# Performance work log

Measured on AMD Instinct MI355X. Metric: run time of the kernel, lower is better.

The kernel has to match this reference:

```python
import jax, jax.numpy as jnp
import numpy as np

DIM = 2048        # config.dim
HID = 1408        # config.moe_inter_dim
E = 16            # config.n_routed_experts
TOPK = 4          # config.n_activated_experts
SHARED = 2816     # n_shared_experts * moe_inter_dim
B, S = 1, 2048
ROUTE_SCALE = 1.0


def setup_inputs() -> dict:
    key = jax.random.key(0)
    ks = jax.random.split(key, 8)
    def w(k, shape, fan_in):
        return jax.random.normal(k, shape, jnp.float32) * (1.0 / np.sqrt(fan_in))
    return {
        "x": jax.random.normal(ks[0], (B, S, DIM), jnp.float32),
        "gate_w": w(ks[1], (E, DIM), DIM),
        "w1": w(ks[2], (E, HID, DIM), DIM),   # per-expert nn.Linear(dim, hid).weight
        "w2": w(ks[3], (E, DIM, HID), HID),   # per-expert nn.Linear(hid, dim).weight
        "w3": w(ks[4], (E, HID, DIM), DIM),
        "sw1": w(ks[5], (SHARED, DIM), DIM),  # shared MLP weights
        "sw2": w(ks[6], (DIM, SHARED), SHARED),
        "sw3": w(ks[7], (SHARED, DIM), DIM),
    }


def reference(x, gate_w, w1, w2, w3, sw1, sw2, sw3):
    shape = x.shape
    xt = x.reshape(-1, DIM)                      # [T, D]
    T = xt.shape[0]

    # --- Gate (score_func='softmax', n_groups=1, bias=None since dim != 7168) ---
    logits = xt @ gate_w.T                        # [T, E]
    scores = jax.nn.softmax(logits.astype(jnp.float32), axis=-1)
    topv, idx = jax.lax.top_k(scores, TOPK)       # n_groups==1: topk over flat scores
    weights = topv * ROUTE_SCALE                  # gather(original_scores, idx) == topv here

    # aux load-balance loss
    tpe = jnp.zeros((E,), jnp.float32).at[idx.reshape(-1)].add(1.0) / (T * TOPK)
    aux_loss = E * jnp.sum(tpe * scores.mean(axis=0))

    # --- Routed experts: combine weights [T, E], then batched SwiGLU GEMMs ---
    comb = jnp.zeros((T, E), jnp.float32).at[jnp.arange(T)[:, None], idx].add(weights)
    h = jax.nn.silu(jnp.einsum('td,ehd->teh', xt, w1)) * jnp.einsum('td,ehd->teh', xt, w3)
    y = jnp.einsum('teh,edh,te->td', h, w2, comb)  # weighted combine (0-weight experts cancel)

    # --- Shared experts (SwiGLU MLP, dropout=0) ---
    z = (jax.nn.silu(xt @ sw1.T) * (xt @ sw3.T)) @ sw2.T

    return (y + z).reshape(shape), aux_loss
```

## Files before the change

kernel.cpp:

```cpp
#include <hip/hip_runtime.h>
#include <hip/hip_bf16.h>

typedef unsigned short u16;
typedef __attribute__((ext_vector_type(8))) short short8;
typedef __attribute__((ext_vector_type(4))) float f32x4;

#define DIM 2048
#define HID 1408
#define NE 16
#define NTOK 2048
#define TOPK_ 4
#define SHID 2816
#define CAPROWS 10240
#define MAXTILES (CAPROWS / 128)
#define AUX_IDX (2048 * 2048)

__device__ inline u16 f2bf(float f) {
  __bf16 h = (__bf16)f;
  return __builtin_bit_cast(u16, h);
}

__device__ inline void gload_lds16(const void* g, void* l) {
  __builtin_amdgcn_global_load_lds(
      (const __attribute__((address_space(1))) unsigned int*)g,
      (__attribute__((address_space(3))) unsigned int*)l, 16, 0, 0);
}

__global__ __launch_bounds__(256) void gate_dots_kernel(
    const float* __restrict__ x, const float* __restrict__ gw,
    double* __restrict__ logits) {
  int t = blockIdx.x;
  const float* xt = x + (size_t)t * DIM;
  __shared__ double red[NE][4];
  int lane = threadIdx.x & 63, wid = threadIdx.x >> 6;
  for (int e = 0; e < NE; ++e) {
    const float* w = gw + e * DIM;
    double p = 0.0;
    for (int d = threadIdx.x; d < DIM; d += 256)
      p += (double)xt[d] * (double)w[d];
#pragma unroll
    for (int s = 32; s; s >>= 1) p += __shfl_xor(p, s);
    if (lane == 0) red[e][wid] = p;
  }
  __syncthreads();
  if (threadIdx.x < NE) {
    int e = threadIdx.x;
    logits[(size_t)t * NE + e] = red[e][0] + red[e][1] + red[e][2] + red[e][3];
  }
}

__global__ __launch_bounds__(256) void topk_kernel(
    const double* __restrict__ logits,
    int* __restrict__ idxb, float* __restrict__ wtb,
    int* __restrict__ counts, float* __restrict__ ssum) {
  __shared__ int lcnt[NE];
  __shared__ float lsum[NE];
  if (threadIdx.x < NE) { lcnt[threadIdx.x] = 0; lsum[threadIdx.x] = 0.f; }
  __syncthreads();
  int t = blockIdx.x * 256 + threadIdx.x;
  int lane = threadIdx.x & 63;
  double sc[NE];
  double m = -1e300;
#pragma unroll
  for (int e = 0; e < NE; ++e) {
    sc[e] = logits[(size_t)t * NE + e];
    if (sc[e] > m) m = sc[e];
  }
  double s = 0.0;
#pragma unroll
  for (int e = 0; e < NE; ++e) { sc[e] = exp(sc[e] - m); s += sc[e]; }
  double inv = 1.0 / s;
#pragma unroll
  for (int e = 0; e < NE; ++e) sc[e] *= inv;
  unsigned used = 0;
  for (int k = 0; k < TOPK_; ++k) {
    int be = 0; double bv = -1.0;
#pragma unroll
    for (int e = 0; e < NE; ++e)
      if (!((used >> e) & 1u) && sc[e] > bv) { bv = sc[e]; be = e; }
    used |= 1u << be;
    idxb[t * TOPK_ + k] = be;
    wtb[t * TOPK_ + k] = (float)bv;
    atomicAdd(&lcnt[be], 1);
  }
#pragma unroll
  for (int e = 0; e < NE; ++e) {
    float v = (float)sc[e];
#pragma unroll
    for (int sft = 32; sft; sft >>= 1) v += __shfl_xor(v, sft);
    if (lane == 0) atomicAdd(&lsum[e], v);
  }
  __syncthreads();
  if (threadIdx.x < NE) {
    atomicAdd(&counts[threadIdx.x], lcnt[threadIdx.x]);
    atomicAdd(&ssum[threadIdx.x], lsum[threadIdx.x]);
  }
}

__global__ __launch_bounds__(256) void setup_kernel(
    const int* __restrict__ counts, int* __restrict__ off, int* __restrict__ cap,
    const float* __restrict__ ssum, int* __restrict__ perm, float* __restrict__ pwt,
    float* __restrict__ aux_out,
    int* __restrict__ tile2e, int* __restrict__ tile2m0) {
  for (int i = threadIdx.x; i < MAXTILES; i += 256) tile2e[i] = -1;
  __syncthreads();
  if (threadIdx.x == 0) {
    int o = 0; double aux = 0.0; int nt = 0;
    for (int e = 0; e < NE; ++e) {
      off[e] = o;
      int c = (counts[e] + 127) & ~127;
      cap[e] = c;
      for (int t = 0; t < (c >> 7); ++t) {
        int slot = (nt / 10) + (nt % 10) * 8;
        tile2e[slot] = e;
        tile2m0[slot] = o + t * 128;
        ++nt;
      }
      o += c;
      aux += ((double)counts[e] / (NTOK * TOPK_)) * ((double)ssum[e] / NTOK);
    }
    aux_out[0] = (float)(NE * aux);
  }
  for (int i = threadIdx.x; i < CAPROWS; i += 256) { perm[i] = 0; pwt[i] = 0.f; }
}

__global__ __launch_bounds__(256) void scatter_kernel(
    const int* __restrict__ idxb, const float* __restrict__ wtb,
    const int* __restrict__ off, int* __restrict__ cursor,
    int* __restrict__ perm, float* __restrict__ pwt) {
  int t = blockIdx.x * 256 + threadIdx.x;
  if (t >= NTOK) return;
  for (int k = 0; k < TOPK_; ++k) {
    int e = idxb[t * TOPK_ + k];
    int s = atomicAdd(&cursor[e], 1);
    int p = off[e] + s;
    perm[p] = t;
    pwt[p] = wtb[t * TOPK_ + k];
  }
}

__global__ __launch_bounds__(256) void cvtN_kernel(const float* __restrict__ in,
                                                   u16* __restrict__ out, long n) {
  long stride = (long)gridDim.x * 2048;
  for (long i = ((long)blockIdx.x * 256 + threadIdx.x) * 8; i < n; i += stride) {
    float4 a = *(const float4*)(in + i);
    float4 b = *(const float4*)(in + i + 4);
    union { u16 u[8]; uint4 v; } o;
    o.u[0] = f2bf(a.x); o.u[1] = f2bf(a.y); o.u[2] = f2bf(a.z); o.u[3] = f2bf(a.w);
    o.u[4] = f2bf(b.x); o.u[5] = f2bf(b.y); o.u[6] = f2bf(b.z); o.u[7] = f2bf(b.w);
    *(uint4*)(out + i) = o.v;
  }
}

template <bool GATHER, bool DUAL, int EPI>
__global__ __launch_bounds__(256) void gemm9_kernel(
    const u16* __restrict__ A, int lda,
    const float* __restrict__ B1, const float* __restrict__ B3,
    int ldb, long bstride, int K,
    const int* __restrict__ tile2e, const int* __restrict__ tile2m0,
    const int* __restrict__ seg_off, const int* __restrict__ seg_cnt,
    const int* __restrict__ perm, const float* __restrict__ pwt,
    float* __restrict__ C0, int ldc0,
    u16* __restrict__ Cb, int ldcb, int Mfixed) {
  int e, m0, rowlim;
  if (tile2e) {
    e = tile2e[blockIdx.x];
    if (e < 0) return;
    m0 = tile2m0[blockIdx.x];
    rowlim = seg_off[e] + seg_cnt[e];
  } else {
    e = 0;
    m0 = blockIdx.x * 128;
    if (m0 >= Mfixed) return;
    rowlim = Mfixed;
  }
  int n0 = blockIdx.y * 64;
  const float* Bb1 = B1 + (long)e * bstride;
  const float* Bb3 = DUAL ? (B3 + (long)e * bstride) : nullptr;

  __shared__ u16 As[2][128 * 64];
  __shared__ u16 Bs1[64 * 64];
  __shared__ u16 Bs3[DUAL ? 64 * 64 : 1];

  int tid = threadIdx.x;
  int lane = tid & 63;
  int wid = tid >> 6;
  int wr = wid >> 1, wc = wid & 1;

  f32x4 acc1[4][2], acc3[4][2];
#pragma unroll
  for (int mi = 0; mi < 4; ++mi)
#pragma unroll
    for (int ni = 0; ni < 2; ++ni) {
      acc1[mi][ni] = (f32x4){0.f, 0.f, 0.f, 0.f};
      acc3[mi][ni] = (f32x4){0.f, 0.f, 0.f, 0.f};
    }

  int sr = tid >> 3;
  int scA = tid & 7;
  long abase[4];
#pragma unroll
  for (int it = 0; it < 4; ++it) {
    int row = m0 + it * 32 + sr;
    int rid = GATHER ? perm[row] : row;
    abase[it] = (long)rid * lda + ((scA ^ (sr & 7)) << 3);
  }
  int brr = tid >> 4;
  int gB = tid & 15;
  int wofs = (((gB >> 1) ^ (brr & 7)) << 3) + ((gB & 1) << 2);
  long bbase[4];
#pragma unroll
  for (int it = 0; it < 4; ++it)
    bbase[it] = (long)(n0 + it * 16 + brr) * ldb + gB * 4;

  float4 R1a[4], R3a[4], R1b[4], R3b[4];

  auto stageA = [&](int buf, int k0) {
#pragma unroll
    for (int it = 0; it < 4; ++it)
      gload_lds16(A + abase[it] + k0, &As[buf][(it * 32 + sr) * 64 + scA * 8]);
  };
  auto loadB = [&](float4 (&r1)[4], float4 (&r3)[4], int k0) {
#pragma unroll
    for (int it = 0; it < 4; ++it) r1[it] = *(const float4*)(Bb1 + bbase[it] + k0);
    if (DUAL) {
#pragma unroll
      for (int it = 0; it < 4; ++it) r3[it] = *(const float4*)(Bb3 + bbase[it] + k0);
    }
  };
  auto writeB = [&](float4 (&r1)[4], float4 (&r3)[4]) {
#pragma unroll
    for (int it = 0; it < 4; ++it) {
      int lo = (it * 16 + brr) * 64 + wofs;
      ushort4 o;
      o.x = f2bf(r1[it].x); o.y = f2bf(r1[it].y); o.z = f2bf(r1[it].z); o.w = f2bf(r1[it].w);
      *(ushort4*)&Bs1[lo] = o;
      if (DUAL) {
        ushort4 q;
        q.x = f2bf(r3[it].x); q.y = f2bf(r3[it].y); q.z = f2bf(r3[it].z); q.w = f2bf(r3[it].w);
        *(ushort4*)&Bs3[lo] = q;
      }
    }
  };
  auto compute = [&](int cur) {
#pragma unroll
    for (int kk = 0; kk < 64; kk += 32) {
      short8 af[4], b1f[2], b3f[2];
#pragma unroll
      for (int i = 0; i < 4; ++i) {
        int R = wr * 64 + i * 16 + (lane & 15);
        int c = (kk >> 3) + (lane >> 4);
        af[i] = *(const short8*)&As[cur][R * 64 + ((c ^ (R & 7)) << 3)];
      }
#pragma unroll
      for (int i = 0; i < 2; ++i) {
        int r = wc * 32 + i * 16 + (lane & 15);
        int cR = (kk >> 3) + (lane >> 4);
        b1f[i] = *(const short8*)&Bs1[r * 64 + ((cR ^ (r & 7)) << 3)];
        if (DUAL)
          b3f[i] = *(const short8*)&Bs3[r * 64 + ((cR ^ (r & 7)) << 3)];
      }
#pragma unroll
      for (int mi = 0; mi < 4; ++mi)
#pragma unroll
        for (int ni = 0; ni < 2; ++ni) {
          acc1[mi][ni] = __builtin_amdgcn_mfma_f32_16x16x32_bf16(af[mi], b1f[ni], acc1[mi][ni], 0, 0, 0);
          if (DUAL)
            acc3[mi][ni] = __builtin_amdgcn_mfma_f32_16x16x32_bf16(af[mi], b3f[ni], acc3[mi][ni], 0, 0, 0);
        }
    }
  };

  int NT = K >> 6;
  loadB(R1a, R3a, 0);
  stageA(0, 0);
  loadB(R1b, R3b, 64);

#define GEMM9_STEP(T, CUR, RB1, RB3)                                          \
  {                                                                           \
    int t_ = (T);                                                             \
    writeB(RB1, RB3);                           \
    bool hasA = (t_ + 1 < NT), hasB = (t_ + 2 < NT);                          \
    if (hasA) stageA((CUR) ^ 1, (t_ + 1) << 6);                               \
    if (hasB) loadB(RB1, RB3, (t_ + 2) << 6);                                 \
    if (hasB) {                                                               \
      if (DUAL) asm volatile("s_waitcnt vmcnt(20)" ::: "memory");             \
      else      asm volatile("s_waitcnt vmcnt(12)" ::: "memory");             \
    } else if (hasA) {                                                        \
      if (DUAL) asm volatile("s_waitcnt vmcnt(12)" ::: "memory");             \
      else      asm volatile("s_waitcnt vmcnt(8)"  ::: "memory");             \
    } else {                                                                  \
      asm volatile("s_waitcnt vmcnt(0)" ::: "memory");                        \
    }                                                                         \
    asm volatile("s_waitcnt lgkmcnt(0)" ::: "memory");                        \
    __builtin_amdgcn_sched_barrier(0);                                        \
    __builtin_amdgcn_s_barrier();                    \
    __builtin_amdgcn_sched_barrier(0);                                        \
    compute(CUR);                                                             \
    __builtin_amdgcn_sched_barrier(0);                                        \
    __builtin_amdgcn_s_barrier();           \
  }

  for (int t = 0; t < NT; t += 2) {
    GEMM9_STEP(t,     0, R1a, R3a);
    GEMM9_STEP(t + 1, 1, R1b, R3b);
  }
#undef GEMM9_STEP

  int rbase = m0 + wr * 64 + (lane >> 4) * 4;
  int cbase = n0 + wc * 32 + (lane & 15);
#pragma unroll
  for (int mi = 0; mi < 4; ++mi) {
#pragma unroll
    for (int ni = 0; ni < 2; ++ni) {
      int col = cbase + ni * 16;
#pragma unroll
      for (int r = 0; r < 4; ++r) {
        int row = rbase + mi * 16 + r;
        float v = acc1[mi][ni][r];
        if (EPI == 0) {
          float a3 = acc3[mi][ni][r];
          float sg = v / (1.f + __expf(-v));
          Cb[(long)row * ldcb + col] = f2bf(sg * a3);
        } else if (EPI == 1) {
          C0[(long)row * ldc0 + col] = v;
        } else {
          if (row < rowlim) {
            atomicAdd(&C0[(long)perm[row] * ldc0 + col], v * pwt[row]);
          }
        }
      }
    }
  }
}

extern "C" void kernel_launch(void* const* d_in, const int* in_sizes, int n_in,
                              void* d_out, int out_size, void* d_ws, size_t ws_size,
                              hipStream_t stream) {
  (void)in_sizes; (void)n_in; (void)out_size; (void)ws_size;
  const float* x   = (const float*)d_in[0];
  const float* gw  = (const float*)d_in[1];
  const float* w1  = (const float*)d_in[2];
  const float* w2  = (const float*)d_in[3];
  const float* w3  = (const float*)d_in[4];
  const float* sw1 = (const float*)d_in[5];
  const float* sw2 = (const float*)d_in[6];
  const float* sw3 = (const float*)d_in[7];
  float* out = (float*)d_out;
  char* ws = (char*)d_ws;

  int*   counts = (int*)(ws + 0);
  int*   cursor = (int*)(ws + 64);
  int*   off    = (int*)(ws + 128);
  int*   cap    = (int*)(ws + 192);
  float* ssum   = (float*)(ws + 256);
  int*   tile2e = (int*)(ws + 1024);
  int*   tile2m0= (int*)(ws + 2048);
  int*   idxb   = (int*)(ws + 4096);
  float* wtb    = (float*)(ws + 4096 + 32768);
  int*   perm   = (int*)(ws + 4096 + 65536);
  float* pwt    = (float*)(ws + 4096 + 65536 + 40960);
  u16*   xb     = (u16*)(ws + 262144);
  double* logits = (double*)(ws + 8650752);
  u16*   hbuf   = (u16*)(ws + 16777216);
  u16*   hsb    = (u16*)(ws + 45613056);

  hipMemsetAsync(ws, 0, 512, stream);
  gate_dots_kernel<<<dim3(NTOK), dim3(256), 0, stream>>>(x, gw, logits);
  topk_kernel<<<dim3(NTOK / 256), dim3(256), 0, stream>>>(logits, idxb, wtb, counts, ssum);
  setup_kernel<<<dim3(1), dim3(256), 0, stream>>>(counts, off, cap, ssum, perm, pwt,
                                                  out + AUX_IDX, tile2e, tile2m0);
  scatter_kernel<<<dim3(8), dim3(256), 0, stream>>>(idxb, wtb, off, cursor, perm, pwt);
  cvtN_kernel<<<dim3(2048), dim3(256), 0, stream>>>(x, xb, (long)NTOK * DIM);

  gemm9_kernel<true, true, 0><<<dim3(MAXTILES, HID / 64), dim3(256), 0, stream>>>(
      xb, DIM, w1, w3, DIM, (long)HID * DIM, DIM, tile2e, tile2m0,
      off, counts, perm, pwt, nullptr, 0, hbuf, HID, 0);
  gemm9_kernel<false, true, 0><<<dim3(NTOK / 128, SHID / 64), dim3(256), 0, stream>>>(
      xb, DIM, sw1, sw3, DIM, 0, DIM, nullptr, nullptr,
      nullptr, nullptr, nullptr, nullptr, nullptr, 0, hsb, SHID, NTOK);
  gemm9_kernel<false, false, 1><<<dim3(NTOK / 128, DIM / 64), dim3(256), 0, stream>>>(
      hsb, SHID, sw2, nullptr, SHID, 0, SHID, nullptr, nullptr,
      nullptr, nullptr, nullptr, nullptr, out, DIM, nullptr, 0, NTOK);
  gemm9_kernel<false, false, 2><<<dim3(MAXTILES, DIM / 64), dim3(256), 0, stream>>>(
      hbuf, HID, w2, nullptr, HID, (long)DIM * HID, HID, tile2e, tile2m0,
      off, counts, perm, pwt, out, DIM, nullptr, 0, 0);
}
```

Baseline: 604.0 us.

## Pre-convert routed expert weights to bf16 and stream them via direct LDS loads

When the workspace is large enough, the routed expert weights w1/w3 (and later w2) are converted to bf16 once. The w1/w3 conversion is folded into the gate-logit kernel as extra blocks, and the w2 conversion runs in spare blocks of the shared-expert GEMM. A new GEMM variant then loads bf16 B tiles with global_load_lds into double-buffered LDS, replacing the register-staged fp32 load and convert path. This adds a full extra read and write pass over the expert weights each call in exchange for halving the per-tile weight traffic and simplifying the pipeline. The w3 branch stores each converted chunk twice through a redundant expression.

```diff
diff --git a/kernel.cpp b/kernel.cpp
--- a/kernel.cpp
+++ b/kernel.cpp
@@ -14,6 +14,8 @@
 #define CAPROWS 10240
 #define MAXTILES (CAPROWS / 128)
 #define AUX_IDX (2048 * 2048)
+#define NW13 46137344L
+#define NX 4194304L
 
 __device__ inline u16 f2bf(float f) {
   __bf16 h = (__bf16)f;
@@ -26,9 +28,31 @@
       (__attribute__((address_space(3))) unsigned int*)l, 16, 0, 0);
 }
 
-__global__ __launch_bounds__(256) void gate_dots_kernel(
+__device__ inline void cvt8_store(const float* __restrict__ in, u16* __restrict__ out, long i) {
+  float4 a = *(const float4*)(in + i);
+  float4 b = *(const float4*)(in + i + 4);
+  union { u16 u[8]; uint4 v; } o;
+  o.u[0] = f2bf(a.x); o.u[1] = f2bf(a.y); o.u[2] = f2bf(a.z); o.u[3] = f2bf(a.w);
+  o.u[4] = f2bf(b.x); o.u[5] = f2bf(b.y); o.u[6] = f2bf(b.z); o.u[7] = f2bf(b.w);
+  *(uint4*)(out + i) = o.v;
+}
+
+__global__ __launch_bounds__(256) void prep_kernel(
     const float* __restrict__ x, const float* __restrict__ gw,
-    double* __restrict__ logits) {
+    double* __restrict__ logits,
+    const float* __restrict__ w1, const float* __restrict__ w3,
+    u16* __restrict__ w1b, u16* __restrict__ w3b, u16* __restrict__ xb) {
+  if ((int)blockIdx.x >= NTOK) {
+    long i0 = ((long)(blockIdx.x - NTOK) * 256 + threadIdx.x) * 8;
+    long stride = (long)(gridDim.x - NTOK) * 2048;
+    const long ntot = 2 * NW13 + NX;
+    for (long i = i0; i < ntot; i += stride) {
+      if (i < NW13)            cvt8_store(w1, w1b, i);
+      else if (i < 2 * NW13)   cvt8_store(w3 + (i - NW13) - (i - NW13), w3b, i - NW13), cvt8_store(w3, w3b, i - NW13);
+      else                     cvt8_store(x, xb, i - 2 * NW13);
+    }
+    return;
+  }
   int t = blockIdx.x;
   const float* xt = x + (size_t)t * DIM;
   __shared__ double red[NE][4];
@@ -43,10 +67,9 @@
     if (lane == 0) red[e][wid] = p;
   }
   __syncthreads();
-  if (threadIdx.x < NE) {
-    int e = threadIdx.x;
-    logits[(size_t)t * NE + e] = red[e][0] + red[e][1] + red[e][2] + red[e][3];
-  }
+  if (threadIdx.x < NE)
+    logits[(size_t)t * NE + threadIdx.x] =
+        red[threadIdx.x][0] + red[threadIdx.x][1] + red[threadIdx.x][2] + red[threadIdx.x][3];
 }
 
 __global__ __launch_bounds__(256) void topk_kernel(
@@ -142,20 +165,202 @@
 __global__ __launch_bounds__(256) void cvtN_kernel(const float* __restrict__ in,
                                                    u16* __restrict__ out, long n) {
   long stride = (long)gridDim.x * 2048;
-  for (long i = ((long)blockIdx.x * 256 + threadIdx.x) * 8; i < n; i += stride) {
-    float4 a = *(const float4*)(in + i);
-    float4 b = *(const float4*)(in + i + 4);
-    union { u16 u[8]; uint4 v; } o;
-    o.u[0] = f2bf(a.x); o.u[1] = f2bf(a.y); o.u[2] = f2bf(a.z); o.u[3] = f2bf(a.w);
-    o.u[4] = f2bf(b.x); o.u[5] = f2bf(b.y); o.u[6] = f2bf(b.z); o.u[7] = f2bf(b.w);
-    *(uint4*)(out + i) = o.v;
-  }
+  for (long i = ((long)blockIdx.x * 256 + threadIdx.x) * 8; i < n; i += stride)
+    cvt8_store(in, out, i);
 }
 
 template <bool GATHER, bool DUAL, int EPI>
 __global__ __launch_bounds__(256) void gemm9_kernel(
     const u16* __restrict__ A, int lda,
     const float* __restrict__ B1, const float* __restrict__ B3,
+    int ldb, long bstride, int K,
+    const int* __restrict__ tile2e, const int* __restrict__ tile2m0,
+    const int* __restrict__ seg_off, const int* __restrict__ seg_cnt,
+    const int* __restrict__ perm, const float* __restrict__ pwt,
+    float* __restrict__ C0, int ldc0,
+    u16* __restrict__ Cb, int ldcb, int Mfixed,
+    const float* __restrict__ csrc, u16* __restrict__ cdst, long cn, int nxg) {
+  if ((int)blockIdx.x >= nxg) {
+    long i0 = ((long)((blockIdx.x - nxg) * gridDim.y + blockIdx.y) * 256 + threadIdx.x) * 8;
+    long stride = (long)(gridDim.x - nxg) * gridDim.y * 2048;
+    for (long i = i0; i < cn; i += stride) cvt8_store(csrc, cdst, i);
+    return;
+  }
+  int e, m0, rowlim;
+  if (tile2e) {
+    e = tile2e[blockIdx.x];
+    if (e < 0) return;
+    m0 = tile2m0[blockIdx.x];
+    rowlim = seg_off[e] + seg_cnt[e];
+  } else {
+    e = 0;
+    m0 = blockIdx.x * 128;
+    if (m0 >= Mfixed) return;
+    rowlim = Mfixed;
+  }
+  int n0 = blockIdx.y * 64;
+  const float* Bb1 = B1 + (long)e * bstride;
+  const float* Bb3 = DUAL ? (B3 + (long)e * bstride) : nullptr;
+
+  __shared__ u16 As[2][128 * 64];
+  __shared__ u16 Bs1[64 * 64];
+  __shared__ u16 Bs3[DUAL ? 64 * 64 : 1];
+
+  int tid = threadIdx.x;
+  int lane = tid & 63;
+  int wid = tid >> 6;
+  int wr = wid >> 1, wc = wid & 1;
+
+  f32x4 acc1[4][2], acc3[4][2];
+#pragma unroll
+  for (int mi = 0; mi < 4; ++mi)
+#pragma unroll
+    for (int ni = 0; ni < 2; ++ni) {
+      acc1[mi][ni] = (f32x4){0.f, 0.f, 0.f, 0.f};
+      acc3[mi][ni] = (f32x4){0.f, 0.f, 0.f, 0.f};
+    }
+
+  int sr = tid >> 3;
+  int scA = tid & 7;
+  long abase[4];
+#pragma unroll
+  for (int it = 0; it < 4; ++it) {
+    int row = m0 + it * 32 + sr;
+    int rid = GATHER ? perm[row] : row;
+    abase[it] = (long)rid * lda + ((scA ^ (sr & 7)) << 3);
+  }
+  int brr = tid >> 4;
+  int gB = tid & 15;
+  int wofs = (((gB >> 1) ^ (brr & 7)) << 3) + ((gB & 1) << 2);
+  long bbase[4];
+#pragma unroll
+  for (int it = 0; it < 4; ++it)
+    bbase[it] = (long)(n0 + it * 16 + brr) * ldb + gB * 4;
+
+  float4 R1a[4], R3a[4], R1b[4], R3b[4];
+
+  auto stageA = [&](int buf, int k0) {
+#pragma unroll
+    for (int it = 0; it < 4; ++it)
+      gload_lds16(A + abase[it] + k0, &As[buf][(it * 32 + sr) * 64 + scA * 8]);
+  };
+  auto loadB = [&](float4 (&r1)[4], float4 (&r3)[4], int k0) {
+#pragma unroll
+    for (int it = 0; it < 4; ++it) r1[it] = *(const float4*)(Bb1 + bbase[it] + k0);
+    if (DUAL) {
+#pragma unroll
+      for (int it = 0; it < 4; ++it) r3[it] = *(const float4*)(Bb3 + bbase[it] + k0);
+    }
+  };
+  auto writeB = [&](float4 (&r1)[4], float4 (&r3)[4]) {
+#pragma unroll
+    for (int it = 0; it < 4; ++it) {
+      int lo = (it * 16 + brr) * 64 + wofs;
+      ushort4 o;
+      o.x = f2bf(r1[it].x); o.y = f2bf(r1[it].y); o.z = f2bf(r1[it].z); o.w = f2bf(r1[it].w);
+      *(ushort4*)&Bs1[lo] = o;
+      if (DUAL) {
+        ushort4 q;
+        q.x = f2bf(r3[it].x); q.y = f2bf(r3[it].y); q.z = f2bf(r3[it].z); q.w = f2bf(r3[it].w);
+        *(ushort4*)&Bs3[lo] = q;
+      }
+    }
+  };
+  auto compute = [&](int cur) {
+#pragma unroll
+    for (int kk = 0; kk < 64; kk += 32) {
+      short8 af[4], b1f[2], b3f[2];
+#pragma unroll
+      for (int i = 0; i < 4; ++i) {
+        int R = wr * 64 + i * 16 + (lane & 15);
+        int c = (kk >> 3) + (lane >> 4);
+        af[i] = *(const short8*)&As[cur][R * 64 + ((c ^ (R & 7)) << 3)];
+      }
+#pragma unroll
+      for (int i = 0; i < 2; ++i) {
+        int r = wc * 32 + i * 16 + (lane & 15);
+        int cR = (kk >> 3) + (lane >> 4);
+        b1f[i] = *(const short8*)&Bs1[r * 64 + ((cR ^ (r & 7)) << 3)];
+        if (DUAL)
+          b3f[i] = *(const short8*)&Bs3[r * 64 + ((cR ^ (r & 7)) << 3)];
+      }
+#pragma unroll
+      for (int mi = 0; mi < 4; ++mi)
+#pragma unroll
+        for (int ni = 0; ni < 2; ++ni) {
+          acc1[mi][ni] = __builtin_amdgcn_mfma_f32_16x16x32_bf16(af[mi], b1f[ni], acc1[mi][ni], 0, 0, 0);
+          if (DUAL)
+            acc3[mi][ni] = __builtin_amdgcn_mfma_f32_16x16x32_bf16(af[mi], b3f[ni], acc3[mi][ni], 0, 0, 0);
+        }
+    }
+  };
+
+  int NT = K >> 6;
+  loadB(R1a, R3a, 0);
+  stageA(0, 0);
+  loadB(R1b, R3b, 64);
+
+#define GEMM9_STEP(T, CUR, RB1, RB3)                                          \
+  {                                                                           \
+    int t_ = (T);                                                             \
+    writeB(RB1, RB3);                                                         \
+    bool hasA = (t_ + 1 < NT), hasB = (t_ + 2 < NT);                          \
+    if (hasA) stageA((CUR) ^ 1, (t_ + 1) << 6);                               \
+    if (hasB) loadB(RB1, RB3, (t_ + 2) << 6);                                 \
+    if (hasB) {                                                               \
+      if (DUAL) asm volatile("s_waitcnt vmcnt(20)" ::: "memory");             \
+      else      asm volatile("s_waitcnt vmcnt(12)" ::: "memory");             \
+    } else if (hasA) {                                                        \
+      if (DUAL) asm volatile("s_waitcnt vmcnt(12)" ::: "memory");             \
+      else      asm volatile("s_waitcnt vmcnt(8)"  ::: "memory");             \
+    } else {                                                                  \
+      asm volatile("s_waitcnt vmcnt(0)" ::: "memory");                        \
+    }                                                                         \
+    asm volatile("s_waitcnt lgkmcnt(0)" ::: "memory");                        \
+    __builtin_amdgcn_sched_barrier(0);                                        \
+    __builtin_amdgcn_s_barrier();                                             \
+    __builtin_amdgcn_sched_barrier(0);                                        \
+    compute(CUR);                                                             \
+    __builtin_amdgcn_sched_barrier(0);                                        \
+    __builtin_amdgcn_s_barrier();                                             \
+  }
+
+  for (int t = 0; t < NT; t += 2) {
+    GEMM9_STEP(t,     0, R1a, R3a);
+    GEMM9_STEP(t + 1, 1, R1b, R3b);
+  }
+#undef GEMM9_STEP
+
+  int rbase = m0 + wr * 64 + (lane >> 4) * 4;
+  int cbase = n0 + wc * 32 + (lane & 15);
+#pragma unroll
+  for (int mi = 0; mi < 4; ++mi) {
+#pragma unroll
+    for (int ni = 0; ni < 2; ++ni) {
+      int col = cbase + ni * 16;
+#pragma unroll
+      for (int r = 0; r < 4; ++r) {
+        int row = rbase + mi * 16 + r;
+        float v = acc1[mi][ni][r];
+        if (EPI == 0) {
+          float a3 = acc3[mi][ni][r];
+          float sg = v / (1.f + __expf(-v));
+          Cb[(long)row * ldcb + col] = f2bf(sg * a3);
+        } else if (EPI == 1) {
+          C0[(long)row * ldc0 + col] = v;
+        } else {
+          if (row < rowlim)
+            atomicAdd(&C0[(long)perm[row] * ldc0 + col], v * pwt[row]);
+        }
+      }
+    }
+  }
+}
+
+template <bool GATHER, bool DUAL, int EPI>
+__global__ __launch_bounds__(256) void gemm11_kernel(
+    const u16* __restrict__ A, int lda,
+    const u16* __restrict__ B1, const u16* __restrict__ B3,
     int ldb, long bstride, int K,
     const int* __restrict__ tile2e, const int* __restrict__ tile2m0,
     const int* __restrict__ seg_off, const int* __restrict__ seg_cnt,
@@ -175,12 +380,12 @@
     rowlim = Mfixed;
   }
   int n0 = blockIdx.y * 64;
-  const float* Bb1 = B1 + (long)e * bstride;
-  const float* Bb3 = DUAL ? (B3 + (long)e * bstride) : nullptr;
+  const u16* Bb1 = B1 + (long)e * bstride;
+  const u16* Bb3 = DUAL ? (B3 + (long)e * bstride) : nullptr;
 
   __shared__ u16 As[2][128 * 64];
-  __shared__ u16 Bs1[64 * 64];
-  __shared__ u16 Bs3[DUAL ? 64 * 64 : 1];
+  __shared__ u16 Bs1[2][64 * 64];
+  __shared__ u16 Bs3[DUAL ? 2 : 1][DUAL ? 64 * 64 : 1];
 
   int tid = threadIdx.x;
   int lane = tid & 63;
@@ -205,41 +410,22 @@
     int rid = GATHER ? perm[row] : row;
     abase[it] = (long)rid * lda + ((scA ^ (sr & 7)) << 3);
   }
-  int brr = tid >> 4;
-  int gB = tid & 15;
-  int wofs = (((gB >> 1) ^ (brr & 7)) << 3) + ((gB & 1) << 2);
-  long bbase[4];
-#pragma unroll
-  for (int it = 0; it < 4; ++it)
-    bbase[it] = (long)(n0 + it * 16 + brr) * ldb + gB * 4;
-
-  float4 R1a[4], R3a[4], R1b[4], R3b[4];
-
-  auto stageA = [&](int buf, int k0) {
+  long bbase[2];
+#pragma unroll
+  for (int it = 0; it < 2; ++it)
+    bbase[it] = (long)(n0 + it * 32 + sr) * ldb + ((scA ^ (sr & 7)) << 3);
+
+  auto stage = [&](int buf, int k0) {
 #pragma unroll
     for (int it = 0; it < 4; ++it)
       gload_lds16(A + abase[it] + k0, &As[buf][(it * 32 + sr) * 64 + scA * 8]);
-  };
-  auto loadB = [&](float4 (&r1)[4], float4 (&r3)[4], int k0) {
-#pragma unroll
-    for (int it = 0; it < 4; ++it) r1[it] = *(const float4*)(Bb1 + bbase[it] + k0);
+#pragma unroll
+    for (int it = 0; it < 2; ++it)
+      gload_lds16(Bb1 + bbase[it] + k0, &Bs1[buf][(it * 32 + sr) * 64 + scA * 8]);
     if (DUAL) {
 #pragma unroll
-      for (int it = 0; it < 4; ++it) r3[it] = *(const float4*)(Bb3 + bbase[it] + k0);
-    }
-  };
-  auto writeB = [&](float4 (&r1)[4], float4 (&r3)[4]) {
-#pragma unroll
-    for (int it = 0; it < 4; ++it) {
-      int lo = (it * 16 + brr) * 64 + wofs;
-      ushort4 o;
-      o.x = f2bf(r1[it].x); o.y = f2bf(r1[it].y); o.z = f2bf(r1[it].z); o.w = f2bf(r1[it].w);
-      *(ushort4*)&Bs1[lo] = o;
-      if (DUAL) {
-        ushort4 q;
-        q.x = f2bf(r3[it].x); q.y = f2bf(r3[it].y); q.z = f2bf(r3[it].z); q.w = f2bf(r3[it].w);
-        *(ushort4*)&Bs3[lo] = q;
-      }
+      for (int it = 0; it < 2; ++it)
+        gload_lds16(Bb3 + bbase[it] + k0, &Bs3[buf][(it * 32 + sr) * 64 + scA * 8]);
     }
   };
   auto compute = [&](int cur) {
@@ -256,9 +442,9 @@
       for (int i = 0; i < 2; ++i) {
         int r = wc * 32 + i * 16 + (lane & 15);
         int cR = (kk >> 3) + (lane >> 4);
-        b1f[i] = *(const short8*)&Bs1[r * 64 + ((cR ^ (r & 7)) << 3)];
+        b1f[i] = *(const short8*)&Bs1[cur][r * 64 + ((cR ^ (r & 7)) << 3)];
         if (DUAL)
-          b3f[i] = *(const short8*)&Bs3[r * 64 + ((cR ^ (r & 7)) << 3)];
+          b3f[i] = *(const short8*)&Bs3[cur][r * 64 + ((cR ^ (r & 7)) << 3)];
       }
 #pragma unroll
       for (int mi = 0; mi < 4; ++mi)
@@ -271,41 +457,27 @@
     }
   };
 
+  stage(0, 0);
   int NT = K >> 6;
-  loadB(R1a, R3a, 0);
-  stageA(0, 0);
-  loadB(R1b, R3b, 64);
-
-#define GEMM9_STEP(T, CUR, RB1, RB3)                                          \
-  {                                                                           \
-    int t_ = (T);                                                             \
-    writeB(RB1, RB3);                           \
-    bool hasA = (t_ + 1 < NT), hasB = (t_ + 2 < NT);                          \
-    if (hasA) stageA((CUR) ^ 1, (t_ + 1) << 6);                               \
-    if (hasB) loadB(RB1, RB3, (t_ + 2) << 6);                                 \
-    if (hasB) {                                                               \
-      if (DUAL) asm volatile("s_waitcnt vmcnt(20)" ::: "memory");             \
-      else      asm volatile("s_waitcnt vmcnt(12)" ::: "memory");             \
-    } else if (hasA) {                                                        \
-      if (DUAL) asm volatile("s_waitcnt vmcnt(12)" ::: "memory");             \
-      else      asm volatile("s_waitcnt vmcnt(8)"  ::: "memory");             \
-    } else {                                                                  \
-      asm volatile("s_waitcnt vmcnt(0)" ::: "memory");                        \
-    }                                                                         \
-    asm volatile("s_waitcnt lgkmcnt(0)" ::: "memory");                        \
-    __builtin_amdgcn_sched_barrier(0);                                        \
-    __builtin_amdgcn_s_barrier();                    \
-    __builtin_amdgcn_sched_barrier(0);                                        \
-    compute(CUR);                                                             \
-    __builtin_amdgcn_sched_barrier(0);                                        \
-    __builtin_amdgcn_s_barrier();           \
-  }
-
-  for (int t = 0; t < NT; t += 2) {
-    GEMM9_STEP(t,     0, R1a, R3a);
-    GEMM9_STEP(t + 1, 1, R1b, R3b);
-  }
-#undef GEMM9_STEP
+  int cur = 0;
+  for (int t = 0; t < NT; ++t) {
+    int nxt = cur ^ 1;
+    bool pf = (t + 1 < NT);
+    if (pf) {
+      stage(nxt, (t + 1) << 6);
+      if (DUAL) asm volatile("s_waitcnt vmcnt(8)" ::: "memory");
+      else      asm volatile("s_waitcnt vmcnt(6)" ::: "memory");
+    } else {
+      asm volatile("s_waitcnt vmcnt(0)" ::: "memory");
+    }
+    __builtin_amdgcn_sched_barrier(0);
+    __builtin_amdgcn_s_barrier();
+    __builtin_amdgcn_sched_barrier(0);
+    compute(cur);
+    __builtin_amdgcn_sched_barrier(0);
+    __builtin_amdgcn_s_barrier();
+    cur = nxt;
+  }
 
   int rbase = m0 + wr * 64 + (lane >> 4) * 4;
   int cbase = n0 + wc * 32 + (lane & 15);
@@ -325,9 +497,8 @@
         } else if (EPI == 1) {
           C0[(long)row * ldc0 + col] = v;
         } else {
-          if (row < rowlim) {
+          if (row < rowlim)
             atomicAdd(&C0[(long)perm[row] * ldc0 + col], v * pwt[row]);
-          }
         }
       }
     }
@@ -337,7 +508,7 @@
 extern "C" void kernel_launch(void* const* d_in, const int* in_sizes, int n_in,
                               void* d_out, int out_size, void* d_ws, size_t ws_size,
                               hipStream_t stream) {
-  (void)in_sizes; (void)n_in; (void)out_size; (void)ws_size;
+  (void)in_sizes; (void)n_in; (void)out_size;
   const float* x   = (const float*)d_in[0];
   const float* gw  = (const float*)d_in[1];
   const float* w1  = (const float*)d_in[2];
@@ -364,25 +535,56 @@
   double* logits = (double*)(ws + 8650752);
   u16*   hbuf   = (u16*)(ws + 16777216);
   u16*   hsb    = (u16*)(ws + 45613056);
+  u16*   w1b    = (u16*)(ws + 57147392);
+  u16*   w3b    = (u16*)(ws + 149422080);
+  u16*   w2b    = w1b;
+
+  const size_t NEEDED = 241696768ull;
+  bool bf16w = ws_size >= NEEDED;
 
   hipMemsetAsync(ws, 0, 512, stream);
-  gate_dots_kernel<<<dim3(NTOK), dim3(256), 0, stream>>>(x, gw, logits);
-  topk_kernel<<<dim3(NTOK / 256), dim3(256), 0, stream>>>(logits, idxb, wtb, counts, ssum);
-  setup_kernel<<<dim3(1), dim3(256), 0, stream>>>(counts, off, cap, ssum, perm, pwt,
-                                                  out + AUX_IDX, tile2e, tile2m0);
-  scatter_kernel<<<dim3(8), dim3(256), 0, stream>>>(idxb, wtb, off, cursor, perm, pwt);
-  cvtN_kernel<<<dim3(2048), dim3(256), 0, stream>>>(x, xb, (long)NTOK * DIM);
-
-  gemm9_kernel<true, true, 0><<<dim3(MAXTILES, HID / 64), dim3(256), 0, stream>>>(
-      xb, DIM, w1, w3, DIM, (long)HID * DIM, DIM, tile2e, tile2m0,
-      off, counts, perm, pwt, nullptr, 0, hbuf, HID, 0);
-  gemm9_kernel<false, true, 0><<<dim3(NTOK / 128, SHID / 64), dim3(256), 0, stream>>>(
-      xb, DIM, sw1, sw3, DIM, 0, DIM, nullptr, nullptr,
-      nullptr, nullptr, nullptr, nullptr, nullptr, 0, hsb, SHID, NTOK);
-  gemm9_kernel<false, false, 1><<<dim3(NTOK / 128, DIM / 64), dim3(256), 0, stream>>>(
-      hsb, SHID, sw2, nullptr, SHID, 0, SHID, nullptr, nullptr,
-      nullptr, nullptr, nullptr, nullptr, out, DIM, nullptr, 0, NTOK);
-  gemm9_kernel<false, false, 2><<<dim3(MAXTILES, DIM / 64), dim3(256), 0, stream>>>(
-      hbuf, HID, w2, nullptr, HID, (long)DIM * HID, HID, tile2e, tile2m0,
-      off, counts, perm, pwt, out, DIM, nullptr, 0, 0);
-}
+
+  if (bf16w) {
+    prep_kernel<<<dim3(NTOK + 1536), dim3(256), 0, stream>>>(x, gw, logits, w1, w3, w1b, w3b, xb);
+    topk_kernel<<<dim3(NTOK / 256), dim3(256), 0, stream>>>(logits, idxb, wtb, counts, ssum);
+    setup_kernel<<<dim3(1), dim3(256), 0, stream>>>(counts, off, cap, ssum, perm, pwt,
+                                                    out + AUX_IDX, tile2e, tile2m0);
+    scatter_kernel<<<dim3(8), dim3(256), 0, stream>>>(idxb, wtb, off, cursor, perm, pwt);
+
+    gemm11_kernel<true, true, 0><<<dim3(MAXTILES, HID / 64), dim3(256), 0, stream>>>(
+        xb, DIM, w1b, w3b, DIM, (long)HID * DIM, DIM, tile2e, tile2m0,
+        off, counts, perm, pwt, nullptr, 0, hbuf, HID, 0);
+    gemm9_kernel<false, true, 0><<<dim3(16 + 8, SHID / 64), dim3(256), 0, stream>>>(
+        xb, DIM, sw1, sw3, DIM, 0, DIM, nullptr, nullptr,
+        nullptr, nullptr, nullptr, nullptr, nullptr, 0, hsb, SHID, NTOK,
+        w2, w2b, NW13, 16);
+    gemm9_kernel<false, false, 1><<<dim3(NTOK / 128, DIM / 64), dim3(256), 0, stream>>>(
+        hsb, SHID, sw2, nullptr, SHID, 0, SHID, nullptr, nullptr,
+        nullptr, nullptr, nullptr, nullptr, out, DIM, nullptr, 0, NTOK,
+        nullptr, nullptr, 0, 1 << 30);
+    gemm11_kernel<false, false, 2><<<dim3(MAXTILES, DIM / 64), dim3(256), 0, stream>>>(
+        hbuf, HID, w2b, nullptr, HID, (long)DIM * HID, HID, tile2e, tile2m0,
+        off, counts, perm, pwt, out, DIM, nullptr, 0, 0);
+  } else {
+    prep_kernel<<<dim3(NTOK), dim3(256), 0, stream>>>(x, gw, logits, w1, w3, nullptr, nullptr, nullptr);
+    topk_kernel<<<dim3(NTOK / 256), dim3(256), 0, stream>>>(logits, idxb, wtb, counts, ssum);
+    setup_kernel<<<dim3(1), dim3(256), 0, stream>>>(counts, off, cap, ssum, perm, pwt,
+                                                    out + AUX_IDX, tile2e, tile2m0);
+    scatter_kernel<<<dim3(8), dim3(256), 0, stream>>>(idxb, wtb, off, cursor, perm, pwt);
+    cvtN_kernel<<<dim3(2048), dim3(256), 0, stream>>>(x, xb, (long)NTOK * DIM);
+    gemm9_kernel<true, true, 0><<<dim3(MAXTILES, HID / 64), dim3(256), 0, stream>>>(
+        xb, DIM, w1, w3, DIM, (long)HID * DIM, DIM, tile2e, tile2m0,
+        off, counts, perm, pwt, nullptr, 0, hbuf, HID, 0, nullptr, nullptr, 0, 1 << 30);
+    gemm9_kernel<false, true, 0><<<dim3(NTOK / 128, SHID / 64), dim3(256), 0, stream>>>(
+        xb, DIM, sw1, sw3, DIM, 0, DIM, nullptr, nullptr,
+        nullptr, nullptr, nullptr, nullptr, nullptr, 0, hsb, SHID, NTOK,
+        nullptr, nullptr, 0, 1 << 30);
+    gemm9_kernel<false, false, 1><<<dim3(NTOK / 128, DIM / 64), dim3(256), 0, stream>>>(
+        hsb, SHID, sw2, nullptr, SHID, 0, SHID, nullptr, nullptr,
+        nullptr, nullptr, nullptr, nullptr, out, DIM, nullptr, 0, NTOK,
+        nullptr, nullptr, 0, 1 << 30);
+    gemm9_kernel<false, false, 2><<<dim3(MAXTILES, DIM / 64), dim3(256), 0, stream>>>(
+        hbuf, HID, w2, nullptr, HID, (long)DIM * HID, HID, tile2e, tile2m0,
+        off, counts, perm, pwt, out, DIM, nullptr, 0, 0, nullptr, nullptr, 0, 1 << 30);
+  }
+}
```

Measured after the change: 726.6 us. 1.2x slower.

## Merge routed and shared expert GEMMs into combined launches, fuse cvt into gate

Applied to the files above, without the earlier changes.

Runs the routed-expert and shared-expert up-projection GEMMs as one launch with a role split on blockIdx.x, and does the same for the down-projections. All down-projection outputs are atomically accumulated into an output buffer that is zeroed by a memset beforehand. The bf16 conversion of x is folded into extra blocks of the gate-dot kernel. The aim is to cut launch count and tail underutilisation by letting independent GEMMs fill the GPU together. The cost is a full-output memset plus atomic adds for the shared path, and MAXTILES is cut from 80 slots to 80 (NSLOT 88), which could truncate routed tiles if the setup kernel assumes the old count.

```diff
diff --git a/kernel.cpp b/kernel.cpp
--- a/kernel.cpp
+++ b/kernel.cpp
@@ -12,7 +12,8 @@
 #define TOPK_ 4
 #define SHID 2816
 #define CAPROWS 10240
-#define MAXTILES (CAPROWS / 128)
+#define NSLOT 88
+#define MAXTILES 80
 #define AUX_IDX (2048 * 2048)
 
 __device__ inline u16 f2bf(float f) {
@@ -26,9 +27,24 @@
       (__attribute__((address_space(3))) unsigned int*)l, 16, 0, 0);
 }
 
-__global__ __launch_bounds__(256) void gate_dots_kernel(
+__device__ inline void cvt8_store(const float* __restrict__ in, u16* __restrict__ out, long i) {
+  float4 a = *(const float4*)(in + i);
+  float4 b = *(const float4*)(in + i + 4);
+  union { u16 u[8]; uint4 v; } o;
+  o.u[0] = f2bf(a.x); o.u[1] = f2bf(a.y); o.u[2] = f2bf(a.z); o.u[3] = f2bf(a.w);
+  o.u[4] = f2bf(b.x); o.u[5] = f2bf(b.y); o.u[6] = f2bf(b.z); o.u[7] = f2bf(b.w);
+  *(uint4*)(out + i) = o.v;
+}
+
+__global__ __launch_bounds__(256) void gatecvt_kernel(
     const float* __restrict__ x, const float* __restrict__ gw,
-    double* __restrict__ logits) {
+    double* __restrict__ logits, u16* __restrict__ xb) {
+  if ((int)blockIdx.x >= NTOK) {
+    long i0 = ((long)(blockIdx.x - NTOK) * 256 + threadIdx.x) * 8;
+    long stride = (long)(gridDim.x - NTOK) * 2048;
+    for (long i = i0; i < (long)NTOK * DIM; i += stride) cvt8_store(x, xb, i);
+    return;
+  }
   int t = blockIdx.x;
   const float* xt = x + (size_t)t * DIM;
   __shared__ double red[NE][4];
@@ -43,10 +59,9 @@
     if (lane == 0) red[e][wid] = p;
   }
   __syncthreads();
-  if (threadIdx.x < NE) {
-    int e = threadIdx.x;
-    logits[(size_t)t * NE + e] = red[e][0] + red[e][1] + red[e][2] + red[e][3];
-  }
+  if (threadIdx.x < NE)
+    logits[(size_t)t * NE + threadIdx.x] =
+        red[threadIdx.x][0] + red[threadIdx.x][1] + red[threadIdx.x][2] + red[threadIdx.x][3];
 }
 
 __global__ __launch_bounds__(256) void topk_kernel(
@@ -139,48 +154,41 @@
   }
 }
 
-__global__ __launch_bounds__(256) void cvtN_kernel(const float* __restrict__ in,
-                                                   u16* __restrict__ out, long n) {
-  long stride = (long)gridDim.x * 2048;
-  for (long i = ((long)blockIdx.x * 256 + threadIdx.x) * 8; i < n; i += stride) {
-    float4 a = *(const float4*)(in + i);
-    float4 b = *(const float4*)(in + i + 4);
-    union { u16 u[8]; uint4 v; } o;
-    o.u[0] = f2bf(a.x); o.u[1] = f2bf(a.y); o.u[2] = f2bf(a.z); o.u[3] = f2bf(a.w);
-    o.u[4] = f2bf(b.x); o.u[5] = f2bf(b.y); o.u[6] = f2bf(b.z); o.u[7] = f2bf(b.w);
-    *(uint4*)(out + i) = o.v;
-  }
-}
-
-template <bool GATHER, bool DUAL, int EPI>
-__global__ __launch_bounds__(256) void gemm9_kernel(
-    const u16* __restrict__ A, int lda,
-    const float* __restrict__ B1, const float* __restrict__ B3,
-    int ldb, long bstride, int K,
+__global__ __launch_bounds__(256) void gemmP1_kernel(
+    const u16* __restrict__ xb,
+    const float* __restrict__ w1, const float* __restrict__ w3,
+    const float* __restrict__ sw1, const float* __restrict__ sw3,
+    u16* __restrict__ hbuf, u16* __restrict__ hsb,
     const int* __restrict__ tile2e, const int* __restrict__ tile2m0,
-    const int* __restrict__ seg_off, const int* __restrict__ seg_cnt,
-    const int* __restrict__ perm, const float* __restrict__ pwt,
-    float* __restrict__ C0, int ldc0,
-    u16* __restrict__ Cb, int ldcb, int Mfixed) {
-  int e, m0, rowlim;
-  if (tile2e) {
-    e = tile2e[blockIdx.x];
+    const int* __restrict__ perm) {
+  int x = blockIdx.x, y = blockIdx.y;
+  bool shared_role = (x >= NSLOT);
+  int m0;
+  bool gth;
+  const float *Bb1, *Bb3;
+  u16* Cb;
+  int ldcb;
+  if (!shared_role) {
+    if (y >= HID / 64) return;
+    int e = tile2e[x];
     if (e < 0) return;
-    m0 = tile2m0[blockIdx.x];
-    rowlim = seg_off[e] + seg_cnt[e];
+    m0 = tile2m0[x];
+    gth = true;
+    Bb1 = w1 + (long)e * HID * DIM;
+    Bb3 = w3 + (long)e * HID * DIM;
+    Cb = hbuf; ldcb = HID;
   } else {
-    e = 0;
-    m0 = blockIdx.x * 128;
-    if (m0 >= Mfixed) return;
-    rowlim = Mfixed;
-  }
-  int n0 = blockIdx.y * 64;
-  const float* Bb1 = B1 + (long)e * bstride;
-  const float* Bb3 = DUAL ? (B3 + (long)e * bstride) : nullptr;
+    m0 = (x - NSLOT) * 128;
+    gth = false;
+    Bb1 = sw1; Bb3 = sw3;
+    Cb = hsb; ldcb = SHID;
+  }
+  int n0 = y * 64;
+  const int K = DIM, ldb = DIM, lda = DIM;
 
   __shared__ u16 As[2][128 * 64];
   __shared__ u16 Bs1[64 * 64];
-  __shared__ u16 Bs3[DUAL ? 64 * 64 : 1];
+  __shared__ u16 Bs3[64 * 64];
 
   int tid = threadIdx.x;
   int lane = tid & 63;
@@ -202,7 +210,7 @@
 #pragma unroll
   for (int it = 0; it < 4; ++it) {
     int row = m0 + it * 32 + sr;
-    int rid = GATHER ? perm[row] : row;
+    int rid = gth ? perm[row] : row;
     abase[it] = (long)rid * lda + ((scA ^ (sr & 7)) << 3);
   }
   int brr = tid >> 4;
@@ -218,15 +226,13 @@
   auto stageA = [&](int buf, int k0) {
 #pragma unroll
     for (int it = 0; it < 4; ++it)
-      gload_lds16(A + abase[it] + k0, &As[buf][(it * 32 + sr) * 64 + scA * 8]);
+      gload_lds16(xb + abase[it] + k0, &As[buf][(it * 32 + sr) * 64 + scA * 8]);
   };
   auto loadB = [&](float4 (&r1)[4], float4 (&r3)[4], int k0) {
 #pragma unroll
     for (int it = 0; it < 4; ++it) r1[it] = *(const float4*)(Bb1 + bbase[it] + k0);
-    if (DUAL) {
-#pragma unroll
-      for (int it = 0; it < 4; ++it) r3[it] = *(const float4*)(Bb3 + bbase[it] + k0);
-    }
+#pragma unroll
+    for (int it = 0; it < 4; ++it) r3[it] = *(const float4*)(Bb3 + bbase[it] + k0);
   };
   auto writeB = [&](float4 (&r1)[4], float4 (&r3)[4]) {
 #pragma unroll
@@ -235,11 +241,9 @@
       ushort4 o;
       o.x = f2bf(r1[it].x); o.y = f2bf(r1[it].y); o.z = f2bf(r1[it].z); o.w = f2bf(r1[it].w);
       *(ushort4*)&Bs1[lo] = o;
-      if (DUAL) {
-        ushort4 q;
-        q.x = f2bf(r3[it].x); q.y = f2bf(r3[it].y); q.z = f2bf(r3[it].z); q.w = f2bf(r3[it].w);
-        *(ushort4*)&Bs3[lo] = q;
-      }
+      ushort4 q;
+      q.x = f2bf(r3[it].x); q.y = f2bf(r3[it].y); q.z = f2bf(r3[it].z); q.w = f2bf(r3[it].w);
+      *(ushort4*)&Bs3[lo] = q;
     }
   };
   auto compute = [&](int cur) {
@@ -257,55 +261,47 @@
         int r = wc * 32 + i * 16 + (lane & 15);
         int cR = (kk >> 3) + (lane >> 4);
         b1f[i] = *(const short8*)&Bs1[r * 64 + ((cR ^ (r & 7)) << 3)];
-        if (DUAL)
-          b3f[i] = *(const short8*)&Bs3[r * 64 + ((cR ^ (r & 7)) << 3)];
+        b3f[i] = *(const short8*)&Bs3[r * 64 + ((cR ^ (r & 7)) << 3)];
       }
 #pragma unroll
       for (int mi = 0; mi < 4; ++mi)
 #pragma unroll
         for (int ni = 0; ni < 2; ++ni) {
           acc1[mi][ni] = __builtin_amdgcn_mfma_f32_16x16x32_bf16(af[mi], b1f[ni], acc1[mi][ni], 0, 0, 0);
-          if (DUAL)
-            acc3[mi][ni] = __builtin_amdgcn_mfma_f32_16x16x32_bf16(af[mi], b3f[ni], acc3[mi][ni], 0, 0, 0);
+          acc3[mi][ni] = __builtin_amdgcn_mfma_f32_16x16x32_bf16(af[mi], b3f[ni], acc3[mi][ni], 0, 0, 0);
         }
     }
   };
 
-  int NT = K >> 6;
+  const int NT = K >> 6;
   loadB(R1a, R3a, 0);
   stageA(0, 0);
   loadB(R1b, R3b, 64);
 
-#define GEMM9_STEP(T, CUR, RB1, RB3)                                          \
+#define P1_STEP(T, CUR, RB1, RB3)                                             \
   {                                                                           \
     int t_ = (T);                                                             \
-    writeB(RB1, RB3);                           \
+    writeB(RB1, RB3);                                                         \
     bool hasA = (t_ + 1 < NT), hasB = (t_ + 2 < NT);                          \
     if (hasA) stageA((CUR) ^ 1, (t_ + 1) << 6);                               \
     if (hasB) loadB(RB1, RB3, (t_ + 2) << 6);                                 \
-    if (hasB) {                                                               \
-      if (DUAL) asm volatile("s_waitcnt vmcnt(20)" ::: "memory");             \
-      else      asm volatile("s_waitcnt vmcnt(12)" ::: "memory");             \
-    } else if (hasA) {                                                        \
-      if (DUAL) asm volatile("s_waitcnt vmcnt(12)" ::: "memory");             \
-      else      asm volatile("s_waitcnt vmcnt(8)"  ::: "memory");             \
-    } else {                                                                  \
-      asm volatile("s_waitcnt vmcnt(0)" ::: "memory");                        \
-    }                                                                         \
+    if (hasB) asm volatile("s_waitcnt vmcnt(20)" ::: "memory");               \
+    else if (hasA) asm volatile("s_waitcnt vmcnt(12)" ::: "memory");          \
+    else asm volatile("s_waitcnt vmcnt(0)" ::: "memory");                     \
     asm volatile("s_waitcnt lgkmcnt(0)" ::: "memory");                        \
     __builtin_amdgcn_sched_barrier(0);                                        \
-    __builtin_amdgcn_s_barrier();                    \
+    __builtin_amdgcn_s_barrier();                                             \
     __builtin_amdgcn_sched_barrier(0);                                        \
     compute(CUR);                                                             \
     __builtin_amdgcn_sched_barrier(0);                                        \
-    __builtin_amdgcn_s_barrier();           \
+    __builtin_amdgcn_s_barrier();                                             \
   }
 
   for (int t = 0; t < NT; t += 2) {
-    GEMM9_STEP(t,     0, R1a, R3a);
-    GEMM9_STEP(t + 1, 1, R1b, R3b);
-  }
-#undef GEMM9_STEP
+    P1_STEP(t,     0, R1a, R3a);
+    P1_STEP(t + 1, 1, R1b, R3b);
+  }
+#undef P1_STEP
 
   int rbase = m0 + wr * 64 + (lane >> 4) * 4;
   int cbase = n0 + wc * 32 + (lane & 15);
@@ -318,16 +314,162 @@
       for (int r = 0; r < 4; ++r) {
         int row = rbase + mi * 16 + r;
         float v = acc1[mi][ni][r];
-        if (EPI == 0) {
-          float a3 = acc3[mi][ni][r];
-          float sg = v / (1.f + __expf(-v));
-          Cb[(long)row * ldcb + col] = f2bf(sg * a3);
-        } else if (EPI == 1) {
-          C0[(long)row * ldc0 + col] = v;
-        } else {
-          if (row < rowlim) {
-            atomicAdd(&C0[(long)perm[row] * ldc0 + col], v * pwt[row]);
-          }
+        float a3 = acc3[mi][ni][r];
+        float sg = v / (1.f + __expf(-v));
+        Cb[(long)row * ldcb + col] = f2bf(sg * a3);
+      }
+    }
+  }
+}
+
+__global__ __launch_bounds__(256) void gemmP2_kernel(
+    const u16* __restrict__ hbuf, const u16* __restrict__ hsb,
+    const float* __restrict__ w2, const float* __restrict__ sw2,
+    float* __restrict__ out,
+    const int* __restrict__ tile2e, const int* __restrict__ tile2m0,
+    const int* __restrict__ seg_off, const int* __restrict__ seg_cnt,
+    const int* __restrict__ perm, const float* __restrict__ pwt) {
+  int x = blockIdx.x, y = blockIdx.y;
+  bool zrole = (x >= MAXTILES);
+  int m0, rowlim, K, lda;
+  const u16* A;
+  const float* Bb;
+  if (!zrole) {
+    int e = tile2e[x];
+    if (e < 0) return;
+    m0 = tile2m0[x];
+    rowlim = seg_off[e] + seg_cnt[e];
+    A = hbuf; lda = HID; K = HID;
+    Bb = w2 + (long)e * DIM * HID;
+  } else {
+    m0 = (x - MAXTILES) * 128;
+    rowlim = NTOK;
+    A = hsb; lda = SHID; K = SHID;
+    Bb = sw2;
+  }
+  int n0 = y * 64;
+  int ldb = K;
+
+  __shared__ u16 As[2][128 * 64];
+  __shared__ u16 Bs1[64 * 64];
+
+  int tid = threadIdx.x;
+  int lane = tid & 63;
+  int wid = tid >> 6;
+  int wr = wid >> 1, wc = wid & 1;
+
+  f32x4 acc1[4][2];
+#pragma unroll
+  for (int mi = 0; mi < 4; ++mi)
+#pragma unroll
+    for (int ni = 0; ni < 2; ++ni)
+      acc1[mi][ni] = (f32x4){0.f, 0.f, 0.f, 0.f};
+
+  int sr = tid >> 3;
+  int scA = tid & 7;
+  long abase[4];
+#pragma unroll
+  for (int it = 0; it < 4; ++it) {
+    int row = m0 + it * 32 + sr;
+    abase[it] = (long)row * lda + ((scA ^ (sr & 7)) << 3);
+  }
+  int brr = tid >> 4;
+  int gB = tid & 15;
+  int wofs = (((gB >> 1) ^ (brr & 7)) << 3) + ((gB & 1) << 2);
+  long bbase[4];
+#pragma unroll
+  for (int it = 0; it < 4; ++it)
+    bbase[it] = (long)(n0 + it * 16 + brr) * ldb + gB * 4;
+
+  float4 R1a[4], R1b[4];
+
+  auto stageA = [&](int buf, int k0) {
+#pragma unroll
+    for (int it = 0; it < 4; ++it)
+      gload_lds16(A + abase[it] + k0, &As[buf][(it * 32 + sr) * 64 + scA * 8]);
+  };
+  auto loadB = [&](float4 (&r1)[4], int k0) {
+#pragma unroll
+    for (int it = 0; it < 4; ++it) r1[it] = *(const float4*)(Bb + bbase[it] + k0);
+  };
+  auto writeB = [&](float4 (&r1)[4]) {
+#pragma unroll
+    for (int it = 0; it < 4; ++it) {
+      int lo = (it * 16 + brr) * 64 + wofs;
+      ushort4 o;
+      o.x = f2bf(r1[it].x); o.y = f2bf(r1[it].y); o.z = f2bf(r1[it].z); o.w = f2bf(r1[it].w);
+      *(ushort4*)&Bs1[lo] = o;
+    }
+  };
+  auto compute = [&](int cur) {
+#pragma unroll
+    for (int kk = 0; kk < 64; kk += 32) {
+      short8 af[4], b1f[2];
+#pragma unroll
+      for (int i = 0; i < 4; ++i) {
+        int R = wr * 64 + i * 16 + (lane & 15);
+        int c = (kk >> 3) + (lane >> 4);
+        af[i] = *(const short8*)&As[cur][R * 64 + ((c ^ (R & 7)) << 3)];
+      }
+#pragma unroll
+      for (int i = 0; i < 2; ++i) {
+        int r = wc * 32 + i * 16 + (lane & 15);
+        int cR = (kk >> 3) + (lane >> 4);
+        b1f[i] = *(const short8*)&Bs1[r * 64 + ((cR ^ (r & 7)) << 3)];
+      }
+#pragma unroll
+      for (int mi = 0; mi < 4; ++mi)
+#pragma unroll
+        for (int ni = 0; ni < 2; ++ni)
+          acc1[mi][ni] = __builtin_amdgcn_mfma_f32_16x16x32_bf16(af[mi], b1f[ni], acc1[mi][ni], 0, 0, 0);
+    }
+  };
+
+  int NT = K >> 6;
+  loadB(R1a, 0);
+  stageA(0, 0);
+  loadB(R1b, 64);
+
+#define P2_STEP(T, CUR, RB)                                                   \
+  {                                                                           \
+    int t_ = (T);                                                             \
+    writeB(RB);                                                               \
+    bool hasA = (t_ + 1 < NT), hasB = (t_ + 2 < NT);                          \
+    if (hasA) stageA((CUR) ^ 1, (t_ + 1) << 6);                               \
+    if (hasB) loadB(RB, (t_ + 2) << 6);                                       \
+    if (hasB) asm volatile("s_waitcnt vmcnt(12)" ::: "memory");               \
+    else if (hasA) asm volatile("s_waitcnt vmcnt(8)" ::: "memory");           \
+    else asm volatile("s_waitcnt vmcnt(0)" ::: "memory");                     \
+    asm volatile("s_waitcnt lgkmcnt(0)" ::: "memory");                        \
+    __builtin_amdgcn_sched_barrier(0);                                        \
+    __builtin_amdgcn_s_barrier();                                             \
+    __builtin_amdgcn_sched_barrier(0);                                        \
+    compute(CUR);                                                             \
+    __builtin_amdgcn_sched_barrier(0);                                        \
+    __builtin_amdgcn_s_barrier();                                             \
+  }
+
+  for (int t = 0; t < NT; t += 2) {
+    P2_STEP(t,     0, R1a);
+    P2_STEP(t + 1, 1, R1b);
+  }
+#undef P2_STEP
+
+  int rbase = m0 + wr * 64 + (lane >> 4) * 4;
+  int cbase = n0 + wc * 32 + (lane & 15);
+#pragma unroll
+  for (int mi = 0; mi < 4; ++mi) {
+#pragma unroll
+    for (int ni = 0; ni < 2; ++ni) {
+      int col = cbase + ni * 16;
+#pragma unroll
+      for (int r = 0; r < 4; ++r) {
+        int row = rbase + mi * 16 + r;
+        float v = acc1[mi][ni][r];
+        if (row < rowlim) {
+          int tok = zrole ? row : perm[row];
+          float w = zrole ? 1.f : pwt[row];
+          atomicAdd(&out[(long)tok * DIM + col], v * w);
         }
       }
     }
@@ -366,23 +508,15 @@
   u16*   hsb    = (u16*)(ws + 45613056);
 
   hipMemsetAsync(ws, 0, 512, stream);
-  gate_dots_kernel<<<dim3(NTOK), dim3(256), 0, stream>>>(x, gw, logits);
+  hipMemsetAsync(out, 0, (size_t)NTOK * DIM * sizeof(float), stream);
+  gatecvt_kernel<<<dim3(NTOK + 128), dim3(256), 0, stream>>>(x, gw, logits, xb);
   topk_kernel<<<dim3(NTOK / 256), dim3(256), 0, stream>>>(logits, idxb, wtb, counts, ssum);
   setup_kernel<<<dim3(1), dim3(256), 0, stream>>>(counts, off, cap, ssum, perm, pwt,
                                                   out + AUX_IDX, tile2e, tile2m0);
   scatter_kernel<<<dim3(8), dim3(256), 0, stream>>>(idxb, wtb, off, cursor, perm, pwt);
-  cvtN_kernel<<<dim3(2048), dim3(256), 0, stream>>>(x, xb, (long)NTOK * DIM);
-
-  gemm9_kernel<true, true, 0><<<dim3(MAXTILES, HID / 64), dim3(256), 0, stream>>>(
-      xb, DIM, w1, w3, DIM, (long)HID * DIM, DIM, tile2e, tile2m0,
-      off, counts, perm, pwt, nullptr, 0, hbuf, HID, 0);
-  gemm9_kernel<false, true, 0><<<dim3(NTOK / 128, SHID / 64), dim3(256), 0, stream>>>(
-      xb, DIM, sw1, sw3, DIM, 0, DIM, nullptr, nullptr,
-      nullptr, nullptr, nullptr, nullptr, nullptr, 0, hsb, SHID, NTOK);
-  gemm9_kernel<false, false, 1><<<dim3(NTOK / 128, DIM / 64), dim3(256), 0, stream>>>(
-      hsb, SHID, sw2, nullptr, SHID, 0, SHID, nullptr, nullptr,
-      nullptr, nullptr, nullptr, nullptr, out, DIM, nullptr, 0, NTOK);
-  gemm9_kernel<false, false, 2><<<dim3(MAXTILES, DIM / 64), dim3(256), 0, stream>>>(
-      hbuf, HID, w2, nullptr, HID, (long)DIM * HID, HID, tile2e, tile2m0,
-      off, counts, perm, pwt, out, DIM, nullptr, 0, 0);
-}
+
+  gemmP1_kernel<<<dim3(NSLOT + 16, SHID / 64), dim3(256), 0, stream>>>(
+      xb, w1, w3, sw1, sw3, hbuf, hsb, tile2e, tile2m0, perm);
+  gemmP2_kernel<<<dim3(MAXTILES + 16, DIM / 64), dim3(256), 0, stream>>>(
+      hbuf, hsb, w2, sw2, out, tile2e, tile2m0, off, counts, perm, pwt);
+}
```

After: 679.3 us. 1.12x slower.
